# Kernel tuning notes

Hardware: AMD Instinct MI355X
Metric: run time of the kernel (lower is better)

The kernel has to match this reference:

```python
import jax, jax.numpy as jnp
import numpy as np
from jax import lax

SCALE = 2
K_UP = 5


def conv2d(x, w, pad):
    return lax.conv_general_dilated(
        x, w, window_strides=(1, 1), padding=[(pad, pad), (pad, pad)],
        dimension_numbers=("NCHW", "OIHW", "NCHW"))


def bn(x, gamma, beta, mean, var, eps=1e-5):
    # eval-mode batchnorm, per-channel (NCHW)
    inv = gamma / jnp.sqrt(var + eps)
    return x * inv[None, :, None, None] + (beta - mean * inv)[None, :, None, None]


def pixel_shuffle(x, r):
    b, crr, h, w = x.shape
    c = crr // (r * r)
    x = x.reshape(b, c, r, r, h, w)
    x = x.transpose(0, 1, 4, 2, 5, 3)  # b, c, h, r, w, r
    return x.reshape(b, c, h * r, w * r)


def setup_inputs():
    key = jax.random.key(0)
    k0, k1, k2 = jax.random.split(key, 3)
    b, c, h, w = 2, 256, 64, 64
    cmid, cenc = 64, (SCALE * K_UP) ** 2  # 64, 100
    return {
        "X": jax.random.normal(k0, (b, c, h, w), jnp.float32),
        "comp_w": jax.random.normal(k1, (cmid, c, 1, 1), jnp.float32) * 0.05,
        "comp_gamma": jnp.ones((cmid,), jnp.float32),
        "comp_beta": jnp.zeros((cmid,), jnp.float32),
        "comp_mean": jnp.zeros((cmid,), jnp.float32),
        "comp_var": jnp.ones((cmid,), jnp.float32),
        "enc_w": jax.random.normal(k2, (cenc, cmid, 3, 3), jnp.float32) * 0.05,
        "enc_gamma": jnp.ones((cenc,), jnp.float32),
        "enc_beta": jnp.zeros((cenc,), jnp.float32),
        "enc_mean": jnp.zeros((cenc,), jnp.float32),
        "enc_var": jnp.ones((cenc,), jnp.float32),
        "power_p": jnp.ones((1,), jnp.float32),
    }


def reference(X, comp_w, comp_gamma, comp_beta, comp_mean, comp_var,
              enc_w, enc_gamma, enc_beta, enc_mean, enc_var, power_p):
    b, c, h, w = X.shape
    h_, w_ = h * SCALE, w * SCALE

    # kernel prediction branch
    W = conv2d(X, comp_w, 0)
    W = jax.nn.relu(bn(W, comp_gamma, comp_beta, comp_mean, comp_var))
    W = conv2d(W, enc_w, 1)
    W = bn(W, enc_gamma, enc_beta, enc_mean, enc_var)  # no relu
    W = pixel_shuffle(W, SCALE)  # (b, k_up^2, h_, w_)

    # power-normalized softmax: W = softmax(clamp(W)^clamp(p)) over taps
    i = jnp.clip(power_p, 1e-5)  # PowerIndex -> learnable scalar exponent
    W = jnp.clip(W, 1e-5)
    W = jnp.power(W, i[0])
    W = jax.nn.softmax(W, axis=1)

    # content branch: nearest upsample then dilated unfold (k=5, dil=2, pad=4)
    Xu = jnp.repeat(jnp.repeat(X, SCALE, axis=2), SCALE, axis=3)  # (b,c,h_,w_)
    pad = (K_UP // 2) * SCALE  # 4
    Xp = jnp.pad(Xu, ((0, 0), (0, 0), (pad, pad), (pad, pad)))
    patches = jnp.stack(
        [Xp[:, :, ki * SCALE: ki * SCALE + h_, kj * SCALE: kj * SCALE + w_]
         for ki in range(K_UP) for kj in range(K_UP)], axis=2)  # (b,c,25,h_,w_)

    return jnp.einsum("bkhw,bckhw->bchw", W, patches)
```

## Files before the change

### kernel.cpp

```cpp
#include <hip/hip_runtime.h>
#include <math.h>

#define NPX 4096
#define H2 128
#define W2 128
#define PP 66

__global__ __launch_bounds__(256) void k1_conv1x1(
    const float* __restrict__ X, const float* __restrict__ w,
    const float* __restrict__ g, const float* __restrict__ bt,
    const float* __restrict__ m, const float* __restrict__ var,
    float* __restrict__ mid_p)
{
    __shared__ float red[3 * 8 * 64];
    int tid = threadIdx.x;
    int x = tid & 63;
    int ciq = __builtin_amdgcn_readfirstlane(tid >> 6);
    int bx = blockIdx.x;
    int bb = bx >> 6, y = bx & 63;
    int co0 = blockIdx.y * 8;
    int ci0 = ciq * 64;

    const float* xp = X + ((size_t)(bb * 256 + ci0)) * NPX + y * 64 + x;
    const float* wp = w + (size_t)co0 * 256 + ci0;

    float acc[8];
    #pragma unroll
    for (int j = 0; j < 8; ++j) acc[j] = 0.f;

    #pragma unroll 4
    for (int ci = 0; ci < 64; ++ci) {
        float xv = xp[(size_t)ci * NPX];
        #pragma unroll
        for (int j = 0; j < 8; ++j)
            acc[j] += xv * wp[j * 256 + ci];
    }

    if (ciq > 0) {
        #pragma unroll
        for (int j = 0; j < 8; ++j)
            red[((ciq - 1) * 8 + j) * 64 + x] = acc[j];
    }
    __syncthreads();
    if (ciq == 0) {
        #pragma unroll
        for (int j = 0; j < 8; ++j) {
            float a = acc[j] + red[(0 * 8 + j) * 64 + x]
                             + red[(1 * 8 + j) * 64 + x]
                             + red[(2 * 8 + j) * 64 + x];
            int co = co0 + j;
            float inv = g[co] * rsqrtf(var[co] + 1e-5f);
            a = fmaxf(a * inv + (bt[co] - m[co] * inv), 0.f);
            mid_p[((size_t)(bb * 64 + co) * PP + (y + 1)) * PP + (x + 1)] = a;
        }
    }
}

__global__ __launch_bounds__(256) void k2a_conv3x3(
    const float* __restrict__ mid_p, const float* __restrict__ ew,
    float* __restrict__ enc)
{
    __shared__ float red[3 * 20 * 64];
    int tid = threadIdx.x;
    int x = tid & 63;
    int ciq = __builtin_amdgcn_readfirstlane(tid >> 6);
    int bx = blockIdx.x;
    int bb = bx >> 6, y = bx & 63;
    int co0 = blockIdx.y * 20;

    float acc[20];
    #pragma unroll
    for (int j = 0; j < 20; ++j) acc[j] = 0.f;

    const float* wb = ew + ((size_t)co0 * 64 + ciq * 16) * 9;

    #pragma unroll 2
    for (int ci = 0; ci < 16; ++ci) {
        const float* P = mid_p + (((size_t)(bb * 64 + ciq * 16 + ci)) * PP + y) * PP + x;
        float v0 = P[0],       v1 = P[1],       v2 = P[2];
        float v3 = P[PP],      v4 = P[PP + 1],  v5 = P[PP + 2];
        float v6 = P[2 * PP],  v7 = P[2 * PP + 1], v8 = P[2 * PP + 2];
        const float* wp = wb + ci * 9;
        #pragma unroll
        for (int j = 0; j < 20; ++j) {
            const float* wj = wp + j * 576;
            acc[j] += v0 * wj[0] + v1 * wj[1] + v2 * wj[2]
                    + v3 * wj[3] + v4 * wj[4] + v5 * wj[5]
                    + v6 * wj[6] + v7 * wj[7] + v8 * wj[8];
        }
    }

    if (ciq > 0) {
        #pragma unroll
        for (int j = 0; j < 20; ++j)
            red[((ciq - 1) * 20 + j) * 64 + x] = acc[j];
    }
    __syncthreads();
    if (ciq == 0) {
        #pragma unroll
        for (int j = 0; j < 20; ++j) {
            float a = acc[j] + red[(0 * 20 + j) * 64 + x]
                             + red[(1 * 20 + j) * 64 + x]
                             + red[(2 * 20 + j) * 64 + x];
            enc[((size_t)bb * 100 + co0 + j) * NPX + y * 64 + x] = a;
        }
    }
}

__global__ __launch_bounds__(64) void k2b_softmax(
    const float* __restrict__ enc,
    const float* __restrict__ g, const float* __restrict__ bt,
    const float* __restrict__ m, const float* __restrict__ var,
    const float* __restrict__ power_p,
    float* __restrict__ wn)
{
    int s = blockIdx.x & 3;
    int p = (blockIdx.x >> 2) * 64 + threadIdx.x;
    int bb = p >> 12, sp = p & (NPX - 1);
    float pw = fmaxf(power_p[0], 1e-5f);
    float tv[25];
    float mx = -1e30f;
    #pragma unroll
    for (int k = 0; k < 25; ++k) {
        int co = 4 * k + s;
        float inv = g[co] * rsqrtf(var[co] + 1e-5f);
        float e = enc[((size_t)bb * 100 + co) * NPX + sp] * inv + (bt[co] - m[co] * inv);
        e = fmaxf(e, 1e-5f);
        float xq = exp2f(pw * log2f(e));
        tv[k] = xq;
        mx = fmaxf(mx, xq);
    }
    float sum = 0.f;
    #pragma unroll
    for (int k = 0; k < 25; ++k) {
        float e = expf(tv[k] - mx);
        tv[k] = e;
        sum += e;
    }
    float r = 1.0f / sum;
    #pragma unroll
    for (int k = 0; k < 25; ++k)
        wn[((size_t)bb * 100 + s * 25 + k) * NPX + sp] = tv[k] * r;
}

__global__ __launch_bounds__(256) void k3_carafe(
    const float* __restrict__ X, const float* __restrict__ wn,
    float* __restrict__ out)
{
    __shared__ float xt[20 * 520];
    int tid = threadIdx.x;
    int bx = blockIdx.x;
    int bb = bx >> 4;
    int t = bx & 15;
    int ty0 = (t >> 2) * 16, tx0 = (t & 3) * 16;
    int c0 = blockIdx.y * 16;

    int ylq = tid >> 4, xlq = tid & 15;
    int yl = ty0 + ylq, xl = tx0 + xlq;
    int px = yl * 64 + xl;

    float wv[100];
    #pragma unroll
    for (int j = 0; j < 100; ++j)
        wv[j] = wn[((size_t)bb * 100 + j) * NPX + px];

    #pragma unroll
    for (int i = 0; i < 40; ++i) {
        int idx = tid + 256 * i;
        int c = idx & 31;
        int ch = (idx >> 5) & 15;
        int r = idx >> 9;
        int gy = ty0 + r - 2, gx = tx0 + c - 2;
        float val = 0.f;
        if (c < 20 && (unsigned)gy < 64u && (unsigned)gx < 64u)
            val = X[((size_t)(bb * 256 + c0 + ch)) * NPX + gy * 64 + gx];
        xt[r * 520 + ch * 32 + c] = val;
    }
    __syncthreads();

    for (int ch = 0; ch < 16; ++ch) {
        float xv[25];
        #pragma unroll
        for (int ki = 0; ki < 5; ++ki)
            #pragma unroll
            for (int kj = 0; kj < 5; ++kj)
                xv[ki * 5 + kj] = xt[(ylq + ki) * 520 + ch * 32 + (xlq + kj)];
        float a0 = 0.f, a1 = 0.f, a2 = 0.f, a3 = 0.f;
        #pragma unroll
        for (int k = 0; k < 25; ++k) {
            a0 += wv[k]      * xv[k];
            a1 += wv[25 + k] * xv[k];
            a2 += wv[50 + k] * xv[k];
            a3 += wv[75 + k] * xv[k];
        }
        float* ob = out + ((size_t)(bb * 256 + c0 + ch) * H2 + 2 * yl) * W2 + 2 * xl;
        *(float2*)ob        = make_float2(a0, a1);
        *(float2*)(ob + W2) = make_float2(a2, a3);
    }
}

extern "C" void kernel_launch(void* const* d_in, const int* in_sizes, int n_in,
                              void* d_out, int out_size, void* d_ws, size_t ws_size,
                              hipStream_t stream)
{
    const float* X  = (const float*)d_in[0];
    const float* cw = (const float*)d_in[1];
    const float* cg = (const float*)d_in[2];
    const float* cb = (const float*)d_in[3];
    const float* cm = (const float*)d_in[4];
    const float* cv = (const float*)d_in[5];
    const float* ew = (const float*)d_in[6];
    const float* eg = (const float*)d_in[7];
    const float* eb = (const float*)d_in[8];
    const float* em = (const float*)d_in[9];
    const float* ev = (const float*)d_in[10];
    const float* pp = (const float*)d_in[11];
    float* out = (float*)d_out;

    float* ws   = (float*)d_ws;
    float* midp = ws;
    float* enc  = ws + 557568;
    float* wn   = ws + 557568 + 819200;

    hipMemsetAsync(midp, 0, 557568 * sizeof(float), stream);
    k1_conv1x1<<<dim3(128, 8), 256, 0, stream>>>(X, cw, cg, cb, cm, cv, midp);
    k2a_conv3x3<<<dim3(128, 5), 256, 0, stream>>>(midp, ew, enc);
    k2b_softmax<<<dim3(512), 64, 0, stream>>>(enc, eg, eb, em, ev, pp, wn);
    k3_carafe<<<dim3(32, 16), 256, 0, stream>>>(X, wn, out);
}
```

Before: 185.9 us.

## Halve output channels per block in convs and remap CARAFE to row-per-block with wave-per-subpixel

The two convolution kernels now compute half as many output channels per block and launch twice as many blocks, which raises occupancy and parallelism at the cost of re-reading inputs more often. The CARAFE kernel is restructured so that each block handles one input row. Each wave owns one of the four sub-pixel outputs, so a thread holds 25 weights instead of 100. The halo tile is loaded as 5 rows by 72 columns per channel, and the grid grows to four times as many blocks. This cuts register pressure (the 100-weight array) in exchange for more redundant halo loads and scalar, non-vectorized output stores.

```diff
diff --git a/kernel.cpp b/kernel.cpp
--- a/kernel.cpp
+++ b/kernel.cpp
@@ -12,42 +12,40 @@
     const float* __restrict__ m, const float* __restrict__ var,
     float* __restrict__ mid_p)
 {
-    __shared__ float red[3 * 8 * 64];
+    __shared__ float red[3 * 4 * 64];
     int tid = threadIdx.x;
     int x = tid & 63;
     int ciq = __builtin_amdgcn_readfirstlane(tid >> 6);
     int bx = blockIdx.x;
     int bb = bx >> 6, y = bx & 63;
-    int co0 = blockIdx.y * 8;
+    int co0 = blockIdx.y * 4;
     int ci0 = ciq * 64;
 
     const float* xp = X + ((size_t)(bb * 256 + ci0)) * NPX + y * 64 + x;
     const float* wp = w + (size_t)co0 * 256 + ci0;
 
-    float acc[8];
-    #pragma unroll
-    for (int j = 0; j < 8; ++j) acc[j] = 0.f;
-
-    #pragma unroll 4
+    float acc[4] = {0.f, 0.f, 0.f, 0.f};
+
+    #pragma unroll 8
     for (int ci = 0; ci < 64; ++ci) {
         float xv = xp[(size_t)ci * NPX];
         #pragma unroll
-        for (int j = 0; j < 8; ++j)
+        for (int j = 0; j < 4; ++j)
             acc[j] += xv * wp[j * 256 + ci];
     }
 
     if (ciq > 0) {
         #pragma unroll
-        for (int j = 0; j < 8; ++j)
-            red[((ciq - 1) * 8 + j) * 64 + x] = acc[j];
+        for (int j = 0; j < 4; ++j)
+            red[((ciq - 1) * 4 + j) * 64 + x] = acc[j];
     }
     __syncthreads();
     if (ciq == 0) {
         #pragma unroll
-        for (int j = 0; j < 8; ++j) {
-            float a = acc[j] + red[(0 * 8 + j) * 64 + x]
-                             + red[(1 * 8 + j) * 64 + x]
-                             + red[(2 * 8 + j) * 64 + x];
+        for (int j = 0; j < 4; ++j) {
+            float a = acc[j] + red[(0 * 4 + j) * 64 + x]
+                             + red[(1 * 4 + j) * 64 + x]
+                             + red[(2 * 4 + j) * 64 + x];
             int co = co0 + j;
             float inv = g[co] * rsqrtf(var[co] + 1e-5f);
             a = fmaxf(a * inv + (bt[co] - m[co] * inv), 0.f);
@@ -60,29 +58,29 @@
     const float* __restrict__ mid_p, const float* __restrict__ ew,
     float* __restrict__ enc)
 {
-    __shared__ float red[3 * 20 * 64];
+    __shared__ float red[3 * 10 * 64];
     int tid = threadIdx.x;
     int x = tid & 63;
     int ciq = __builtin_amdgcn_readfirstlane(tid >> 6);
     int bx = blockIdx.x;
     int bb = bx >> 6, y = bx & 63;
-    int co0 = blockIdx.y * 20;
-
-    float acc[20];
-    #pragma unroll
-    for (int j = 0; j < 20; ++j) acc[j] = 0.f;
+    int co0 = blockIdx.y * 10;
+
+    float acc[10];
+    #pragma unroll
+    for (int j = 0; j < 10; ++j) acc[j] = 0.f;
 
     const float* wb = ew + ((size_t)co0 * 64 + ciq * 16) * 9;
 
     #pragma unroll 2
     for (int ci = 0; ci < 16; ++ci) {
         const float* P = mid_p + (((size_t)(bb * 64 + ciq * 16 + ci)) * PP + y) * PP + x;
-        float v0 = P[0],       v1 = P[1],       v2 = P[2];
-        float v3 = P[PP],      v4 = P[PP + 1],  v5 = P[PP + 2];
+        float v0 = P[0],       v1 = P[1],          v2 = P[2];
+        float v3 = P[PP],      v4 = P[PP + 1],     v5 = P[PP + 2];
         float v6 = P[2 * PP],  v7 = P[2 * PP + 1], v8 = P[2 * PP + 2];
         const float* wp = wb + ci * 9;
         #pragma unroll
-        for (int j = 0; j < 20; ++j) {
+        for (int j = 0; j < 10; ++j) {
             const float* wj = wp + j * 576;
             acc[j] += v0 * wj[0] + v1 * wj[1] + v2 * wj[2]
                     + v3 * wj[3] + v4 * wj[4] + v5 * wj[5]
@@ -92,16 +90,16 @@
 
     if (ciq > 0) {
         #pragma unroll
-        for (int j = 0; j < 20; ++j)
-            red[((ciq - 1) * 20 + j) * 64 + x] = acc[j];
+        for (int j = 0; j < 10; ++j)
+            red[((ciq - 1) * 10 + j) * 64 + x] = acc[j];
     }
     __syncthreads();
     if (ciq == 0) {
         #pragma unroll
-        for (int j = 0; j < 20; ++j) {
-            float a = acc[j] + red[(0 * 20 + j) * 64 + x]
-                             + red[(1 * 20 + j) * 64 + x]
-                             + red[(2 * 20 + j) * 64 + x];
+        for (int j = 0; j < 10; ++j) {
+            float a = acc[j] + red[(0 * 10 + j) * 64 + x]
+                             + red[(1 * 10 + j) * 64 + x]
+                             + red[(2 * 10 + j) * 64 + x];
             enc[((size_t)bb * 100 + co0 + j) * NPX + y * 64 + x] = a;
         }
     }
@@ -147,55 +145,44 @@
     const float* __restrict__ X, const float* __restrict__ wn,
     float* __restrict__ out)
 {
-    __shared__ float xt[20 * 520];
+    __shared__ float xt[16 * 5 * 72];
     int tid = threadIdx.x;
+    int px = tid & 63;
+    int s = __builtin_amdgcn_readfirstlane(tid >> 6);
+    int dy = s >> 1, dx = s & 1;
     int bx = blockIdx.x;
-    int bb = bx >> 4;
-    int t = bx & 15;
-    int ty0 = (t >> 2) * 16, tx0 = (t & 3) * 16;
+    int bb = bx >> 6, y = bx & 63;
     int c0 = blockIdx.y * 16;
 
-    int ylq = tid >> 4, xlq = tid & 15;
-    int yl = ty0 + ylq, xl = tx0 + xlq;
-    int px = yl * 64 + xl;
-
-    float wv[100];
-    #pragma unroll
-    for (int j = 0; j < 100; ++j)
-        wv[j] = wn[((size_t)bb * 100 + j) * NPX + px];
-
-    #pragma unroll
-    for (int i = 0; i < 40; ++i) {
-        int idx = tid + 256 * i;
-        int c = idx & 31;
-        int ch = (idx >> 5) & 15;
-        int r = idx >> 9;
-        int gy = ty0 + r - 2, gx = tx0 + c - 2;
+    float wv[25];
+    const float* wsrc = wn + ((size_t)bb * 100 + s * 25) * NPX + y * 64 + px;
+    #pragma unroll
+    for (int k = 0; k < 25; ++k)
+        wv[k] = wsrc[(size_t)k * NPX];
+
+    for (int idx = tid; idx < 5760; idx += 256) {
+        int ch = idx / 360;
+        int rem = idx - ch * 360;
+        int r = rem / 72, c = rem - r * 72;
+        int gy = y + r - 2, gx = c - 2;
         float val = 0.f;
-        if (c < 20 && (unsigned)gy < 64u && (unsigned)gx < 64u)
+        if (c < 68 && (unsigned)gy < 64u && (unsigned)gx < 64u)
             val = X[((size_t)(bb * 256 + c0 + ch)) * NPX + gy * 64 + gx];
-        xt[r * 520 + ch * 32 + c] = val;
+        xt[idx] = val;
     }
     __syncthreads();
 
+    int y2 = 2 * y + dy, x2 = 2 * px + dx;
+    float* ob = out + ((size_t)(bb * 256 + c0) * H2 + y2) * W2 + x2;
     for (int ch = 0; ch < 16; ++ch) {
-        float xv[25];
+        const float* xb = &xt[ch * 360 + px];
+        float a = 0.f;
         #pragma unroll
         for (int ki = 0; ki < 5; ++ki)
             #pragma unroll
             for (int kj = 0; kj < 5; ++kj)
-                xv[ki * 5 + kj] = xt[(ylq + ki) * 520 + ch * 32 + (xlq + kj)];
-        float a0 = 0.f, a1 = 0.f, a2 = 0.f, a3 = 0.f;
-        #pragma unroll
-        for (int k = 0; k < 25; ++k) {
-            a0 += wv[k]      * xv[k];
-            a1 += wv[25 + k] * xv[k];
-            a2 += wv[50 + k] * xv[k];
-            a3 += wv[75 + k] * xv[k];
-        }
-        float* ob = out + ((size_t)(bb * 256 + c0 + ch) * H2 + 2 * yl) * W2 + 2 * xl;
-        *(float2*)ob        = make_float2(a0, a1);
-        *(float2*)(ob + W2) = make_float2(a2, a3);
+                a += wv[ki * 5 + kj] * xb[ki * 72 + kj];
+        ob[(size_t)ch * H2 * W2] = a;
     }
 }
 
@@ -223,8 +210,8 @@
     float* wn   = ws + 557568 + 819200;
 
     hipMemsetAsync(midp, 0, 557568 * sizeof(float), stream);
-    k1_conv1x1<<<dim3(128, 8), 256, 0, stream>>>(X, cw, cg, cb, cm, cv, midp);
-    k2a_conv3x3<<<dim3(128, 5), 256, 0, stream>>>(midp, ew, enc);
+    k1_conv1x1<<<dim3(128, 16), 256, 0, stream>>>(X, cw, cg, cb, cm, cv, midp);
+    k2a_conv3x3<<<dim3(128, 10), 256, 0, stream>>>(midp, ew, enc);
     k2b_softmax<<<dim3(512), 64, 0, stream>>>(enc, eg, eb, em, ev, pp, wn);
-    k3_carafe<<<dim3(32, 16), 256, 0, stream>>>(X, wn, out);
-}
+    k3_carafe<<<dim3(128, 16), 256, 0, stream>>>(X, wn, out);
+}
```

Result: faster. 157.3 us (-15.4%).

## Stage weights in LDS, compute two rows per thread, pre-pad X for carafe

Applied to the files above, without the earlier changes.

The 1x1 and 3x3 conv kernels now load their weights into shared memory and each thread computes two output rows. This reuses input loads across rows and replaces repeated global weight reads with LDS reads. The 1x1 kernel also writes a zero-padded copy of X to workspace, so the carafe kernel can read its 5x5 neighbourhoods straight from global memory instead of staging a halo tile in LDS. The cost is a larger memset, an extra 2.3M-float write of X, and global gathers through cache in carafe.

```diff
diff --git a/kernel.cpp b/kernel.cpp
--- a/kernel.cpp
+++ b/kernel.cpp
@@ -5,54 +5,76 @@
 #define H2 128
 #define W2 128
 #define PP 66
+#define XPP 68
 
 __global__ __launch_bounds__(256) void k1_conv1x1(
     const float* __restrict__ X, const float* __restrict__ w,
     const float* __restrict__ g, const float* __restrict__ bt,
     const float* __restrict__ m, const float* __restrict__ var,
-    float* __restrict__ mid_p)
-{
-    __shared__ float red[3 * 8 * 64];
+    float* __restrict__ mid_p, float* __restrict__ Xp)
+{
+    __shared__ float wl[256 * 8];
+    __shared__ float red[3 * 16 * 64];
     int tid = threadIdx.x;
     int x = tid & 63;
     int ciq = __builtin_amdgcn_readfirstlane(tid >> 6);
     int bx = blockIdx.x;
-    int bb = bx >> 6, y = bx & 63;
+    int bb = bx >> 5, y0 = (bx & 31) * 2;
     int co0 = blockIdx.y * 8;
     int ci0 = ciq * 64;
-
-    const float* xp = X + ((size_t)(bb * 256 + ci0)) * NPX + y * 64 + x;
-    const float* wp = w + (size_t)co0 * 256 + ci0;
-
-    float acc[8];
-    #pragma unroll
-    for (int j = 0; j < 8; ++j) acc[j] = 0.f;
-
-    #pragma unroll 4
+    bool dopad = (blockIdx.y == 0);
+
+    for (int idx = tid; idx < 2048; idx += 256) {
+        int ci = idx >> 3, j = idx & 7;
+        wl[idx] = w[(size_t)(co0 + j) * 256 + ci];
+    }
+    __syncthreads();
+
+    float acc[2][8];
+    #pragma unroll
+    for (int r = 0; r < 2; ++r)
+        #pragma unroll
+        for (int j = 0; j < 8; ++j) acc[r][j] = 0.f;
+
+    const float* xp = X + ((size_t)(bb * 256 + ci0)) * NPX + y0 * 64 + x;
+    float* xpad = Xp + ((size_t)(bb * 256 + ci0) * XPP + (y0 + 2)) * XPP + (x + 2);
+
     for (int ci = 0; ci < 64; ++ci) {
-        float xv = xp[(size_t)ci * NPX];
-        #pragma unroll
-        for (int j = 0; j < 8; ++j)
-            acc[j] += xv * wp[j * 256 + ci];
+        float x0 = xp[(size_t)ci * NPX];
+        float x1 = xp[(size_t)ci * NPX + 64];
+        if (dopad) {
+            xpad[(size_t)ci * (XPP * XPP)] = x0;
+            xpad[(size_t)ci * (XPP * XPP) + XPP] = x1;
+        }
+        const float4* wq = (const float4*)&wl[(ci0 + ci) * 8];
+        float4 wa = wq[0], wb = wq[1];
+        acc[0][0] += x0 * wa.x; acc[0][1] += x0 * wa.y; acc[0][2] += x0 * wa.z; acc[0][3] += x0 * wa.w;
+        acc[0][4] += x0 * wb.x; acc[0][5] += x0 * wb.y; acc[0][6] += x0 * wb.z; acc[0][7] += x0 * wb.w;
+        acc[1][0] += x1 * wa.x; acc[1][1] += x1 * wa.y; acc[1][2] += x1 * wa.z; acc[1][3] += x1 * wa.w;
+        acc[1][4] += x1 * wb.x; acc[1][5] += x1 * wb.y; acc[1][6] += x1 * wb.z; acc[1][7] += x1 * wb.w;
     }
 
     if (ciq > 0) {
         #pragma unroll
-        for (int j = 0; j < 8; ++j)
-            red[((ciq - 1) * 8 + j) * 64 + x] = acc[j];
+        for (int r = 0; r < 2; ++r)
+            #pragma unroll
+            for (int j = 0; j < 8; ++j)
+                red[((ciq - 1) * 16 + r * 8 + j) * 64 + x] = acc[r][j];
     }
     __syncthreads();
     if (ciq == 0) {
         #pragma unroll
-        for (int j = 0; j < 8; ++j) {
-            float a = acc[j] + red[(0 * 8 + j) * 64 + x]
-                             + red[(1 * 8 + j) * 64 + x]
-                             + red[(2 * 8 + j) * 64 + x];
-            int co = co0 + j;
-            float inv = g[co] * rsqrtf(var[co] + 1e-5f);
-            a = fmaxf(a * inv + (bt[co] - m[co] * inv), 0.f);
-            mid_p[((size_t)(bb * 64 + co) * PP + (y + 1)) * PP + (x + 1)] = a;
-        }
+        for (int r = 0; r < 2; ++r)
+            #pragma unroll
+            for (int j = 0; j < 8; ++j) {
+                float a = acc[r][j] + red[(0 * 16 + r * 8 + j) * 64 + x]
+                                    + red[(1 * 16 + r * 8 + j) * 64 + x]
+                                    + red[(2 * 16 + r * 8 + j) * 64 + x];
+                int co = co0 + j;
+                float inv = g[co] * rsqrtf(var[co] + 1e-5f);
+                a = fmaxf(a * inv + (bt[co] - m[co] * inv), 0.f);
+                mid_p[((size_t)(bb * 64 + co) * PP + (y0 + r + 1)) * PP + (x + 1)] = a;
+            }
     }
 }
 
@@ -60,50 +82,73 @@
     const float* __restrict__ mid_p, const float* __restrict__ ew,
     float* __restrict__ enc)
 {
+    __shared__ float wl[5760];
     __shared__ float red[3 * 20 * 64];
     int tid = threadIdx.x;
     int x = tid & 63;
     int ciq = __builtin_amdgcn_readfirstlane(tid >> 6);
     int bx = blockIdx.x;
-    int bb = bx >> 6, y = bx & 63;
-    int co0 = blockIdx.y * 20;
-
-    float acc[20];
-    #pragma unroll
-    for (int j = 0; j < 20; ++j) acc[j] = 0.f;
-
-    const float* wb = ew + ((size_t)co0 * 64 + ciq * 16) * 9;
-
-    #pragma unroll 2
+    int bb = bx >> 5, y0 = (bx & 31) * 2;
+    int co0 = blockIdx.y * 10;
+
+    for (int idx = tid; idx < 5760; idx += 256) {
+        int j = idx / 576;
+        int rem = idx - j * 576;
+        int ci = rem / 9, k = rem - ci * 9;
+        wl[ci * 90 + j * 9 + k] = ew[(size_t)(co0 + j) * 576 + rem];
+    }
+    __syncthreads();
+
+    float acc[2][10];
+    #pragma unroll
+    for (int r = 0; r < 2; ++r)
+        #pragma unroll
+        for (int j = 0; j < 10; ++j) acc[r][j] = 0.f;
+
+    const float* P = mid_p + (((size_t)(bb * 64 + ciq * 16)) * PP + y0) * PP + x;
+
     for (int ci = 0; ci < 16; ++ci) {
-        const float* P = mid_p + (((size_t)(bb * 64 + ciq * 16 + ci)) * PP + y) * PP + x;
-        float v0 = P[0],       v1 = P[1],       v2 = P[2];
-        float v3 = P[PP],      v4 = P[PP + 1],  v5 = P[PP + 2];
-        float v6 = P[2 * PP],  v7 = P[2 * PP + 1], v8 = P[2 * PP + 2];
-        const float* wp = wb + ci * 9;
-        #pragma unroll
-        for (int j = 0; j < 20; ++j) {
-            const float* wj = wp + j * 576;
-            acc[j] += v0 * wj[0] + v1 * wj[1] + v2 * wj[2]
-                    + v3 * wj[3] + v4 * wj[4] + v5 * wj[5]
-                    + v6 * wj[6] + v7 * wj[7] + v8 * wj[8];
+        const float* P0 = P + (size_t)ci * (PP * PP);
+        float v[4][3];
+        #pragma unroll
+        for (int r = 0; r < 4; ++r) {
+            v[r][0] = P0[r * PP];
+            v[r][1] = P0[r * PP + 1];
+            v[r][2] = P0[r * PP + 2];
+        }
+        const float* wq = &wl[(ciq * 16 + ci) * 90];
+        #pragma unroll
+        for (int j = 0; j < 10; ++j) {
+            float w0 = wq[j * 9 + 0], w1 = wq[j * 9 + 1], w2 = wq[j * 9 + 2];
+            float w3 = wq[j * 9 + 3], w4 = wq[j * 9 + 4], w5 = wq[j * 9 + 5];
+            float w6 = wq[j * 9 + 6], w7 = wq[j * 9 + 7], w8 = wq[j * 9 + 8];
+            acc[0][j] += v[0][0] * w0 + v[0][1] * w1 + v[0][2] * w2
+                       + v[1][0] * w3 + v[1][1] * w4 + v[1][2] * w5
+                       + v[2][0] * w6 + v[2][1] * w7 + v[2][2] * w8;
+            acc[1][j] += v[1][0] * w0 + v[1][1] * w1 + v[1][2] * w2
+                       + v[2][0] * w3 + v[2][1] * w4 + v[2][2] * w5
+                       + v[3][0] * w6 + v[3][1] * w7 + v[3][2] * w8;
         }
     }
 
     if (ciq > 0) {
         #pragma unroll
-        for (int j = 0; j < 20; ++j)
-            red[((ciq - 1) * 20 + j) * 64 + x] = acc[j];
+        for (int r = 0; r < 2; ++r)
+            #pragma unroll
+            for (int j = 0; j < 10; ++j)
+                red[((ciq - 1) * 20 + r * 10 + j) * 64 + x] = acc[r][j];
     }
     __syncthreads();
     if (ciq == 0) {
         #pragma unroll
-        for (int j = 0; j < 20; ++j) {
-            float a = acc[j] + red[(0 * 20 + j) * 64 + x]
-                             + red[(1 * 20 + j) * 64 + x]
-                             + red[(2 * 20 + j) * 64 + x];
-            enc[((size_t)bb * 100 + co0 + j) * NPX + y * 64 + x] = a;
-        }
+        for (int r = 0; r < 2; ++r)
+            #pragma unroll
+            for (int j = 0; j < 10; ++j) {
+                float a = acc[r][j] + red[(0 * 20 + r * 10 + j) * 64 + x]
+                                    + red[(1 * 20 + r * 10 + j) * 64 + x]
+                                    + red[(2 * 20 + r * 10 + j) * 64 + x];
+                enc[((size_t)bb * 100 + co0 + j) * NPX + (y0 + r) * 64 + x] = a;
+            }
     }
 }
 
@@ -144,47 +189,34 @@
 }
 
 __global__ __launch_bounds__(256) void k3_carafe(
-    const float* __restrict__ X, const float* __restrict__ wn,
+    const float* __restrict__ Xp, const float* __restrict__ wn,
     float* __restrict__ out)
 {
-    __shared__ float xt[20 * 520];
     int tid = threadIdx.x;
     int bx = blockIdx.x;
     int bb = bx >> 4;
-    int t = bx & 15;
-    int ty0 = (t >> 2) * 16, tx0 = (t & 3) * 16;
+    int rg = bx & 15;
+    int y = rg * 4 + (tid >> 6);
+    int px = tid & 63;
     int c0 = blockIdx.y * 16;
 
-    int ylq = tid >> 4, xlq = tid & 15;
-    int yl = ty0 + ylq, xl = tx0 + xlq;
-    int px = yl * 64 + xl;
-
     float wv[100];
+    const float* wsrc = wn + ((size_t)bb * 100) * NPX + y * 64 + px;
     #pragma unroll
     for (int j = 0; j < 100; ++j)
-        wv[j] = wn[((size_t)bb * 100 + j) * NPX + px];
-
-    #pragma unroll
-    for (int i = 0; i < 40; ++i) {
-        int idx = tid + 256 * i;
-        int c = idx & 31;
-        int ch = (idx >> 5) & 15;
-        int r = idx >> 9;
-        int gy = ty0 + r - 2, gx = tx0 + c - 2;
-        float val = 0.f;
-        if (c < 20 && (unsigned)gy < 64u && (unsigned)gx < 64u)
-            val = X[((size_t)(bb * 256 + c0 + ch)) * NPX + gy * 64 + gx];
-        xt[r * 520 + ch * 32 + c] = val;
-    }
-    __syncthreads();
+        wv[j] = wsrc[(size_t)j * NPX];
+
+    const float* xb = Xp + ((size_t)(bb * 256 + c0) * XPP + y) * XPP + px;
+    float* ob = out + ((size_t)(bb * 256 + c0) * H2 + 2 * y) * W2 + 2 * px;
 
     for (int ch = 0; ch < 16; ++ch) {
+        const float* P = xb + (size_t)ch * (XPP * XPP);
         float xv[25];
         #pragma unroll
         for (int ki = 0; ki < 5; ++ki)
             #pragma unroll
             for (int kj = 0; kj < 5; ++kj)
-                xv[ki * 5 + kj] = xt[(ylq + ki) * 520 + ch * 32 + (xlq + kj)];
+                xv[ki * 5 + kj] = P[ki * XPP + kj];
         float a0 = 0.f, a1 = 0.f, a2 = 0.f, a3 = 0.f;
         #pragma unroll
         for (int k = 0; k < 25; ++k) {
@@ -193,9 +225,9 @@
             a2 += wv[50 + k] * xv[k];
             a3 += wv[75 + k] * xv[k];
         }
-        float* ob = out + ((size_t)(bb * 256 + c0 + ch) * H2 + 2 * yl) * W2 + 2 * xl;
-        *(float2*)ob        = make_float2(a0, a1);
-        *(float2*)(ob + W2) = make_float2(a2, a3);
+        float* o = ob + (size_t)ch * (H2 * W2);
+        *(float2*)o        = make_float2(a0, a1);
+        *(float2*)(o + W2) = make_float2(a2, a3);
     }
 }
 
@@ -219,12 +251,13 @@
 
     float* ws   = (float*)d_ws;
     float* midp = ws;
-    float* enc  = ws + 557568;
-    float* wn   = ws + 557568 + 819200;
-
-    hipMemsetAsync(midp, 0, 557568 * sizeof(float), stream);
-    k1_conv1x1<<<dim3(128, 8), 256, 0, stream>>>(X, cw, cg, cb, cm, cv, midp);
-    k2a_conv3x3<<<dim3(128, 5), 256, 0, stream>>>(midp, ew, enc);
+    float* Xp   = ws + 557568;
+    float* enc  = ws + 557568 + 2367488;
+    float* wn   = ws + 557568 + 2367488 + 819200;
+
+    hipMemsetAsync(ws, 0, (557568 + 2367488) * sizeof(float), stream);
+    k1_conv1x1<<<dim3(64, 8), 256, 0, stream>>>(X, cw, cg, cb, cm, cv, midp, Xp);
+    k2a_conv3x3<<<dim3(64, 10), 256, 0, stream>>>(midp, ew, enc);
     k2b_softmax<<<dim3(512), 64, 0, stream>>>(enc, eg, eb, em, ev, pp, wn);
-    k3_carafe<<<dim3(32, 16), 256, 0, stream>>>(X, wn, out);
-}
+    k3_carafe<<<dim3(32, 16), 256, 0, stream>>>(Xp, wn, out);
+}
```

Result: faster. 179.3 us (-3.6%).
